# Performance work log

Measured on AMD Instinct MI355X. Metric: run time of the kernel, lower is better.

## Reference

```python
import jax, jax.numpy as jnp
import numpy as np

MAX_CH = 21
LAT_DIM = 64
D_EMBED = 1024
N_HEADS = 16
D_HEAD = D_EMBED // N_HEADS  # 64
L = MAX_CH * LAT_DIM         # 1344 latents
B, T = 4, 1024


def setup_inputs() -> dict:
    key = jax.random.key(0)
    k1, k2, k3, k4, k5, k6 = jax.random.split(key, 6)
    x = jax.random.normal(k1, (B, T, D_EMBED), dtype=jnp.float32)
    # boolean channel mask [b, L, T]
    ch_mask = jax.random.randint(k2, (B, L, T), 0, 2) > 0
    # learned latent queries [L, H*d] (xavier-uniform-ish init)
    lim_q = float(np.sqrt(6.0 / (L + N_HEADS * D_HEAD)))
    latent_q = jax.random.uniform(k3, (L, N_HEADS * D_HEAD), minval=-lim_q, maxval=lim_q, dtype=jnp.float32)
    # Linear weights (torch layout: [out, in]) and biases
    lim_w = float(np.sqrt(1.0 / D_EMBED))
    w_k_w = jax.random.uniform(k4, (N_HEADS * D_HEAD, D_EMBED), minval=-lim_w, maxval=lim_w, dtype=jnp.float32)
    w_k_b = jnp.zeros((N_HEADS * D_HEAD,), dtype=jnp.float32)
    w_v_w = jax.random.uniform(k5, (N_HEADS * D_HEAD, D_EMBED), minval=-lim_w, maxval=lim_w, dtype=jnp.float32)
    w_v_b = jax.random.uniform(k6, (N_HEADS * D_HEAD,), minval=-lim_w, maxval=lim_w, dtype=jnp.float32)
    return {"x": x, "ch_mask": ch_mask, "latent_q": latent_q,
            "w_k_w": w_k_w, "w_k_b": w_k_b, "w_v_w": w_v_w, "w_v_b": w_v_b}


def reference(x, ch_mask, latent_q, w_k_w, w_k_b, w_v_w, w_v_b):
    b, t, d = x.shape
    H, dh = N_HEADS, D_HEAD
    l = latent_q.shape[0]
    # faithful to torch .view(-1, H, L, d): raw row-major reinterpretation
    lq = latent_q.reshape(1, H, l, dh)                    # [1,H,L,dh]
    k = (x @ w_k_w.T + w_k_b).reshape(b, t, H, dh).transpose(0, 2, 3, 1)  # [b,H,dh,T]
    v = (x @ w_v_w.T + w_v_b).reshape(b, t, H, dh).transpose(0, 2, 1, 3)  # [b,H,T,dh]
    scale = jnp.float32(H) ** -0.5  # note: n_heads**-0.5, as in source
    scores = jnp.einsum('ohld,bhdt->bhlt', lq, k) * scale  # [b,H,L,T]
    mask = ch_mask[:, None, :, :]                           # [b,1,L,T] broadcast over heads
    scores = jnp.where(mask, scores, jnp.float32(-1e9))
    w = jax.nn.softmax(scores, axis=-1)
    w = jnp.where(mask, w, jnp.float32(0.0))
    out = jnp.einsum('bhlt,bhtd->bhld', w, v)               # [b,H,L,dh]
    return out.transpose(0, 2, 1, 3).reshape(b, l, H * dh)  # [b,L,H*dh]
```

## Files before the change

kernel.cpp:

```cpp
#include <hip/hip_runtime.h>
#include <hip/hip_bf16.h>

#define B_SZ 4
#define T_SZ 1024
#define NH 16
#define L_SZ 1344
#define LT_COUNT 21

typedef __attribute__((ext_vector_type(8))) short short8;
typedef __attribute__((ext_vector_type(4))) short short4v;
typedef __attribute__((ext_vector_type(4))) float floatx4;

typedef __attribute__((address_space(1))) const void gvoid;
typedef __attribute__((address_space(3))) void svoid;
#define GLD16(gp, lp) \
  __builtin_amdgcn_global_load_lds((gvoid*)(gp), (svoid*)(lp), 16, 0, 0)

static __device__ inline short bf16bits(float f) {
  return __builtin_bit_cast(short, __float2bfloat16(f));
}
static __device__ inline short4v cvt4(float4 v) {
  short4v r;
  r.x = bf16bits(v.x); r.y = bf16bits(v.y);
  r.z = bf16bits(v.z); r.w = bf16bits(v.w);
  return r;
}

static __device__ inline unsigned pack_bf16_2(float a, float b) {
  unsigned ua = __builtin_bit_cast(unsigned, a) + 0x8000u;
  unsigned ub = __builtin_bit_cast(unsigned, b) + 0x8000u;
  return __builtin_amdgcn_perm(ub, ua, 0x07060302u);
}
static __device__ inline uint2 pack_bf16_4(float4 v) {
  return make_uint2(pack_bf16_2(v.x, v.y), pack_bf16_2(v.z, v.w));
}


__global__ __launch_bounds__(256) void mask_detect(
    const unsigned char* __restrict__ m, int* __restrict__ flag) {
  __shared__ int any_off4, any_at4;
  if (threadIdx.x == 0) { any_off4 = 0; any_at4 = 0; }
  __syncthreads();
  int a1 = 0, a2 = 0;
  for (int i = threadIdx.x; i < 4096; i += 256) {
    unsigned char v = m[i];
    if (v) {
      if ((i & 3) != 0) a1 = 1;
      if ((i & 7) == 4) a2 = 1;
    }
  }
  if (a1) atomicOr(&any_off4, 1);
  if (a2) atomicOr(&any_at4, 1);
  __syncthreads();
  if (threadIdx.x == 0) *flag = any_off4 ? 1 : (any_at4 ? 0 : 2);
}

__global__ __launch_bounds__(256) void maskbits_kernel(
    const void* __restrict__ mask, const int* __restrict__ flag,
    unsigned int* __restrict__ bits) {
  int idx = blockIdx.x * 256 + threadIdx.x;
  int f = *flag;
  bool v;
  if (f == 1)      v = ((const signed char*)mask)[idx] != 0;
  else if (f == 2) v = ((const long long*)mask)[idx] != 0;
  else             v = ((const int*)mask)[idx] != 0;
  unsigned long long bal = __ballot(v);
  int lane = threadIdx.x & 63;
  if ((lane & 31) == 0) {
    unsigned int w = (lane & 32) ? (unsigned int)(bal >> 32) : (unsigned int)bal;
    bits[idx >> 5] = w;
  }
}

__global__ __launch_bounds__(256) void cvt_bf16(
    const float4* __restrict__ src, uint2* __restrict__ dst) {
  size_t i = (size_t)blockIdx.x * 256 + threadIdx.x;
  dst[i] = pack_bf16_4(src[i]);
}

static __device__ __forceinline__ void epi_k(const floatx4 acc[4][4],
    int bxt, int byd, int wm, int wn, int c15, int kq,
    const float* __restrict__ bk, __hip_bfloat16* __restrict__ k_buf) {
  #pragma unroll
  for (int ni = 0; ni < 4; ++ni) {
    int gr = bxt * 128 + wn * 64 + ni * 16 + c15;
    int b = gr >> 10, tc = (gr >> 6) & 15;
    #pragma unroll
    for (int mi = 0; mi < 4; ++mi) {
      int d0 = byd * 128 + wm * 64 + mi * 16 + kq * 4;
      int h = d0 >> 6, hd = d0 & 63;
      int half = hd >> 5, q4 = (hd >> 3) & 3, jlo = hd & 7;
      int bh = b * 16 + h;
      float4 b4 = *(const float4*)(bk + d0);
      float4 v4 = {acc[mi][ni][0] + b4.x, acc[mi][ni][1] + b4.y,
                   acc[mi][ni][2] + b4.z, acc[mi][ni][3] + b4.w};
      *(uint2*)(k_buf + ((size_t)((bh * 16 + tc) * 8 + ni * 2 + half)) * 512 +
                (q4 * 16 + c15) * 8 + jlo) = pack_bf16_4(v4);
    }
  }
}

static __device__ __forceinline__ void epi_v(const floatx4 acc[4][4],
    int bxd, int byt, int wm, int wn, int c15, int kq,
    const float* __restrict__ bv, __hip_bfloat16* __restrict__ v_buf) {
  #pragma unroll
  for (int ni = 0; ni < 4; ++ni) {
    int d = bxd * 128 + wn * 64 + ni * 16 + c15;
    int h = d >> 6;
    float bias = bv[d];
    #pragma unroll
    for (int mi = 0; mi < 4; ++mi) {
      int gr = byt * 128 + wm * 64 + mi * 16 + kq * 4;
      int b = gr >> 10, tc = (gr >> 6) & 15;
      int tl = gr & 63;
      int half = tl >> 5, q4 = (tl >> 3) & 3, jlo = tl & 7;
      int bh = b * 16 + h;
      float4 v4 = {acc[mi][ni][0] + bias, acc[mi][ni][1] + bias,
                   acc[mi][ni][2] + bias, acc[mi][ni][3] + bias};
      *(uint2*)(v_buf + ((size_t)((bh * 16 + tc) * 8 + ni * 2 + half)) * 512 +
                (q4 * 16 + c15) * 8 + jlo) = pack_bf16_4(v4);
    }
  }
}

static __device__ __forceinline__ void gemm_core(
    const __hip_bfloat16* __restrict__ A, const __hip_bfloat16* __restrict__ B,
    __hip_bfloat16* ldsA, __hip_bfloat16* ldsB,
    int TA, int TB, int tid, floatx4 (&acc)[4][4]) {
  const int lane = tid & 63, w = tid >> 6;
  const int wm = w & 1, wn = w >> 1;
  const int c15 = lane & 15, kq = lane >> 4;
  for (int kk = 0; kk < 1024; kk += 32) {
    #pragma unroll
    for (int j = 0; j < 2; ++j) {
      int c = w * 128 + j * 64 + lane;
      int row = c >> 2;
      int gkc = (c & 3) ^ (row & 3);
      GLD16(A + (size_t)(TA * 128 + row) * 1024 + kk + gkc * 8,
            ldsA + (w * 128 + j * 64) * 8);
      GLD16(B + (size_t)(TB * 128 + row) * 1024 + kk + gkc * 8,
            ldsB + (w * 128 + j * 64) * 8);
    }
    __syncthreads();
    short8 af[4], bf[4];
    #pragma unroll
    for (int mi = 0; mi < 4; ++mi) {
      int row = wm * 64 + mi * 16 + c15;
      af[mi] = *(const short8*)(ldsA + row * 32 + ((kq ^ (row & 3)) * 8));
    }
    #pragma unroll
    for (int ni = 0; ni < 4; ++ni) {
      int row = wn * 64 + ni * 16 + c15;
      bf[ni] = *(const short8*)(ldsB + row * 32 + ((kq ^ (row & 3)) * 8));
    }
    #pragma unroll
    for (int mi = 0; mi < 4; ++mi)
      #pragma unroll
      for (int ni = 0; ni < 4; ++ni)
        acc[mi][ni] = __builtin_amdgcn_mfma_f32_16x16x32_bf16(
            af[mi], bf[ni], acc[mi][ni], 0, 0, 0);
    __syncthreads();
  }
}

__global__ __launch_bounds__(256) void gemm_kv_bf16(
    const __hip_bfloat16* __restrict__ xb,
    const __hip_bfloat16* __restrict__ wkb, const __hip_bfloat16* __restrict__ wvb,
    const float* __restrict__ bk, const float* __restrict__ bv,
    __hip_bfloat16* __restrict__ k_buf, __hip_bfloat16* __restrict__ v_buf) {
  __shared__ __align__(16) __hip_bfloat16 ldsA[128 * 32];
  __shared__ __align__(16) __hip_bfloat16 ldsB[128 * 32];
  const int tid = threadIdx.x;
  const int lane = tid & 63, w = tid >> 6;
  const int wm = w & 1, wn = w >> 1;
  const int c15 = lane & 15, kq = lane >> 4;
  floatx4 acc[4][4];
  for (int i = 0; i < 4; ++i)
    for (int j = 0; j < 4; ++j) acc[i][j] = (floatx4){0.f, 0.f, 0.f, 0.f};

  if (blockIdx.z == 0) {
    gemm_core(wkb, xb, ldsA, ldsB, blockIdx.y, blockIdx.x, tid, acc);
    epi_k(acc, blockIdx.x, blockIdx.y, wm, wn, c15, kq, bk, k_buf);
  } else {
    gemm_core(xb, wvb, ldsA, ldsB, blockIdx.x, blockIdx.y, tid, acc);
    epi_v(acc, blockIdx.y, blockIdx.x, wm, wn, c15, kq, bv, v_buf);
  }
}

__global__ __launch_bounds__(256, 3) void attn_kernel(
    const float* __restrict__ latent_q,
    const __hip_bfloat16* __restrict__ k_buf,
    const __hip_bfloat16* __restrict__ v_buf,
    const unsigned int* __restrict__ mbits,
    float* __restrict__ out) {
  __shared__ __align__(16) __hip_bfloat16 ldsK[2][4096];
  __shared__ __align__(16) __hip_bfloat16 ldsV[2][4096];
  __shared__ __align__(16) __hip_bfloat16 pbuf[4][16 * 72];
  __shared__ uint2 mrows[64][17];

  const int tid = threadIdx.x;
  const int lane = tid & 63;
  const int w = tid >> 6;
  int bid = blockIdx.x;
  int xcd = bid & 7, j = bid >> 3;
  int bh = xcd * 8 + j / LT_COUNT;
  int lt = j % LT_COUNT;
  int h = bh & 15, b = bh >> 4;
  const int q4 = lane >> 4, c15 = lane & 15;
  const int l0 = lt * 64;

  {
    const unsigned int* msrc = mbits + (size_t)(b * L_SZ + l0) * 32;
    #pragma unroll
    for (int p = 0; p < 2; ++p) {
      int i = p * 256 + tid;
      uint4 m4 = *(const uint4*)(msrc + i * 4);
      int row = i >> 3, c2 = (i & 7) * 2;
      mrows[row][c2]     = make_uint2(m4.x, m4.y);
      mrows[row][c2 + 1] = make_uint2(m4.z, m4.w);
    }
  }

  const float QS = 0.25f * 1.44269504089f;
  short8 qf[2];
  {
    const float* qp = latent_q + ((size_t)(h * L_SZ + l0 + w * 16 + c15)) * 64 + q4 * 8;
    float4 a0 = *(const float4*)(qp);
    float4 a1 = *(const float4*)(qp + 4);
    float4 a2 = *(const float4*)(qp + 32);
    float4 a3 = *(const float4*)(qp + 36);
    a0.x *= QS; a0.y *= QS; a0.z *= QS; a0.w *= QS;
    a1.x *= QS; a1.y *= QS; a1.z *= QS; a1.w *= QS;
    a2.x *= QS; a2.y *= QS; a2.z *= QS; a2.w *= QS;
    a3.x *= QS; a3.y *= QS; a3.z *= QS; a3.w *= QS;
    short4v t0 = cvt4(a0), t1 = cvt4(a1), t2 = cvt4(a2), t3 = cvt4(a3);
    qf[0] = (short8){t0.x, t0.y, t0.z, t0.w, t1.x, t1.y, t1.z, t1.w};
    qf[1] = (short8){t2.x, t2.y, t2.z, t2.w, t3.x, t3.y, t3.z, t3.w};
  }
  __syncthreads();

  floatx4 l4 = (floatx4){0.f, 0.f, 0.f, 0.f};
  floatx4 o_acc[4];
  #pragma unroll
  for (int di = 0; di < 4; ++di) o_acc[di] = (floatx4){0.f, 0.f, 0.f, 0.f};

  const __hip_bfloat16* kb = k_buf + (size_t)bh * 65536;
  const __hip_bfloat16* vb = v_buf + (size_t)bh * 65536;
  __hip_bfloat16* pw = pbuf[w];

#define STAGE_KV(sb, tcn) do {                                              \
    const __hip_bfloat16* gk_ = kb + (size_t)(tcn) * 4096;                  \
    const __hip_bfloat16* gv_ = vb + (size_t)(tcn) * 4096;                  \
    int o0_ = w * 512 + lane * 8;                                           \
    GLD16(gk_ + o0_,        &ldsK[sb][w * 512]);                            \
    GLD16(gk_ + 2048 + o0_, &ldsK[sb][2048 + w * 512]);                     \
    GLD16(gv_ + o0_,        &ldsV[sb][w * 512]);                            \
    GLD16(gv_ + 2048 + o0_, &ldsV[sb][2048 + w * 512]);                     \
  } while (0)

  STAGE_KV(0, 0);

  for (int tc = 0; tc < 16; ++tc) {
    const int buf = tc & 1;
    if (tc + 1 < 16) {
      STAGE_KV(buf ^ 1, tc + 1);
      asm volatile("s_waitcnt vmcnt(4)" ::: "memory");
    } else {
      asm volatile("s_waitcnt vmcnt(0)" ::: "memory");
    }
    __builtin_amdgcn_s_barrier();

    short8 kf[2][4];
    #pragma unroll
    for (int half = 0; half < 2; ++half)
      #pragma unroll
      for (int ni = 0; ni < 4; ++ni)
        kf[half][ni] = *(const short8*)(&ldsK[buf][(ni * 2 + half) * 512 + lane * 8]);
    uint2 mw = mrows[w * 16 + c15][tc];
    floatx4 s[4];
    #pragma unroll
    for (int ni = 0; ni < 4; ++ni) s[ni] = (floatx4){0.f, 0.f, 0.f, 0.f};
    #pragma unroll
    for (int half = 0; half < 2; ++half)
      #pragma unroll
      for (int ni = 0; ni < 4; ++ni)
        s[ni] = __builtin_amdgcn_mfma_f32_16x16x32_bf16(kf[half][ni], qf[half], s[ni], 0, 0, 0);

    short8 vf[2][4];
    #pragma unroll
    for (int half = 0; half < 2; ++half)
      #pragma unroll
      for (int di = 0; di < 4; ++di)
        vf[half][di] = *(const short8*)(&ldsV[buf][(di * 2 + half) * 512 + lane * 8]);

    #pragma unroll
    for (int ni = 0; ni < 4; ++ni) {
      unsigned mword = (ni >= 2) ? mw.y : mw.x;
      float4 p4;
      #pragma unroll
      for (int r = 0; r < 4; ++r) {
        float e = exp2f(s[ni][r]);
        int sh = (ni & 1) * 16 + q4 * 4 + r;
        ((float*)&p4)[r] = ((mword >> sh) & 1) ? e : 0.f;
      }
      l4[0] += p4.x; l4[1] += p4.y;
      l4[2] += p4.z; l4[3] += p4.w;
      *(uint2*)(pw + c15 * 72 + ni * 16 + q4 * 4) = pack_bf16_4(p4);
    }

    short8 pf0 = *(const short8*)(pw + c15 * 72 + q4 * 8);
    short8 pf1 = *(const short8*)(pw + c15 * 72 + 32 + q4 * 8);
    #pragma unroll
    for (int di = 0; di < 4; ++di)
      o_acc[di] = __builtin_amdgcn_mfma_f32_16x16x32_bf16(vf[0][di], pf0, o_acc[di], 0, 0, 0);
    #pragma unroll
    for (int di = 0; di < 4; ++di)
      o_acc[di] = __builtin_amdgcn_mfma_f32_16x16x32_bf16(vf[1][di], pf1, o_acc[di], 0, 0, 0);

    asm volatile("s_waitcnt lgkmcnt(0)" ::: "memory");
    __builtin_amdgcn_s_barrier();
  }
#undef STAGE_KV

  float la = (l4[0] + l4[1]) + (l4[2] + l4[3]);
  la += __shfl_xor(la, 16, 64);
  la += __shfl_xor(la, 32, 64);
  float inv = (la > 0.f) ? 1.f / la : 0.f;
  float* ob = out + ((size_t)(b * L_SZ + l0 + w * 16 + c15)) * 1024 + h * 64;
  #pragma unroll
  for (int di = 0; di < 4; ++di) {
    float4 o4 = {o_acc[di][0] * inv, o_acc[di][1] * inv,
                 o_acc[di][2] * inv, o_acc[di][3] * inv};
    *(float4*)(ob + di * 16 + q4 * 4) = o4;
  }
}

extern "C" void kernel_launch(void* const* d_in, const int* in_sizes, int n_in,
                              void* d_out, int out_size, void* d_ws, size_t ws_size,
                              hipStream_t stream) {
  const float* x      = (const float*)d_in[0];
  const void* ch_mask = d_in[1];
  const float* lq     = (const float*)d_in[2];
  const float* wk     = (const float*)d_in[3];
  const float* bk     = (const float*)d_in[4];
  const float* wv     = (const float*)d_in[5];
  const float* bv     = (const float*)d_in[6];
  float* out = (float*)d_out;

  char* ws = (char*)d_ws;
  unsigned int* mbits   = (unsigned int*)ws;
  int* flag             = (int*)(ws + 720896);
  __hip_bfloat16* k_buf = (__hip_bfloat16*)(ws + 786432);
  __hip_bfloat16* v_buf = (__hip_bfloat16*)(ws + 786432 + 8388608);

  __hip_bfloat16* xb  = (__hip_bfloat16*)d_out;
  __hip_bfloat16* wkb = xb + 4 * 1024 * 1024;
  __hip_bfloat16* wvb = wkb + 1024 * 1024;

  mask_detect<<<1, 256, 0, stream>>>((const unsigned char*)ch_mask, flag);
  maskbits_kernel<<<21504, 256, 0, stream>>>(ch_mask, flag, mbits);

  cvt_bf16<<<4096, 256, 0, stream>>>((const float4*)x, (uint2*)xb);
  cvt_bf16<<<1024, 256, 0, stream>>>((const float4*)wk, (uint2*)wkb);
  cvt_bf16<<<1024, 256, 0, stream>>>((const float4*)wv, (uint2*)wvb);
  gemm_kv_bf16<<<dim3(32, 8, 2), 256, 0, stream>>>(xb, wkb, wvb, bk, bv, k_buf, v_buf);

  attn_kernel<<<8 * 168, 256, 0, stream>>>(lq, k_buf, v_buf, mbits, out);
}
```

Before: 199.4 us.

## Fuse prep kernels, double-buffer K/V GEMM with smaller tiles, prioritize attention MFMAs

Merges the mask-bit packing and the three bf16 conversion launches into one prep kernel, which removes three kernel launches. Restructures the K/V projection GEMM to use 128x64 tiles with double-buffered LDS staging and a 4-blocks-per-CU launch bound. The smaller tiles give 1024 blocks instead of 512 and let the next k-slice load overlap the current MFMAs. Also raises wave priority around the MFMA sections of the attention kernel with s_setprio. Smaller tiles lower data reuse per block, and the priority hints may shift the instruction schedule unpredictably.

```diff
diff --git a/kernel.cpp b/kernel.cpp
--- a/kernel.cpp
+++ b/kernel.cpp
@@ -55,135 +55,151 @@
   if (threadIdx.x == 0) *flag = any_off4 ? 1 : (any_at4 ? 0 : 2);
 }
 
-__global__ __launch_bounds__(256) void maskbits_kernel(
+__global__ __launch_bounds__(256) void prep_kernel(
+    const float4* __restrict__ x, const float4* __restrict__ wk,
+    const float4* __restrict__ wv,
+    uint2* __restrict__ xb, uint2* __restrict__ wkb, uint2* __restrict__ wvb,
     const void* __restrict__ mask, const int* __restrict__ flag,
     unsigned int* __restrict__ bits) {
-  int idx = blockIdx.x * 256 + threadIdx.x;
-  int f = *flag;
-  bool v;
-  if (f == 1)      v = ((const signed char*)mask)[idx] != 0;
-  else if (f == 2) v = ((const long long*)mask)[idx] != 0;
-  else             v = ((const int*)mask)[idx] != 0;
-  unsigned long long bal = __ballot(v);
-  int lane = threadIdx.x & 63;
-  if ((lane & 31) == 0) {
-    unsigned int w = (lane & 32) ? (unsigned int)(bal >> 32) : (unsigned int)bal;
-    bits[idx >> 5] = w;
-  }
-}
-
-__global__ __launch_bounds__(256) void cvt_bf16(
-    const float4* __restrict__ src, uint2* __restrict__ dst) {
-  size_t i = (size_t)blockIdx.x * 256 + threadIdx.x;
-  dst[i] = pack_bf16_4(src[i]);
-}
-
-static __device__ __forceinline__ void epi_k(const floatx4 acc[4][4],
-    int bxt, int byd, int wm, int wn, int c15, int kq,
-    const float* __restrict__ bk, __hip_bfloat16* __restrict__ k_buf) {
-  #pragma unroll
-  for (int ni = 0; ni < 4; ++ni) {
-    int gr = bxt * 128 + wn * 64 + ni * 16 + c15;
-    int b = gr >> 10, tc = (gr >> 6) & 15;
-    #pragma unroll
-    for (int mi = 0; mi < 4; ++mi) {
-      int d0 = byd * 128 + wm * 64 + mi * 16 + kq * 4;
-      int h = d0 >> 6, hd = d0 & 63;
-      int half = hd >> 5, q4 = (hd >> 3) & 3, jlo = hd & 7;
-      int bh = b * 16 + h;
-      float4 b4 = *(const float4*)(bk + d0);
-      float4 v4 = {acc[mi][ni][0] + b4.x, acc[mi][ni][1] + b4.y,
-                   acc[mi][ni][2] + b4.z, acc[mi][ni][3] + b4.w};
-      *(uint2*)(k_buf + ((size_t)((bh * 16 + tc) * 8 + ni * 2 + half)) * 512 +
-                (q4 * 16 + c15) * 8 + jlo) = pack_bf16_4(v4);
-    }
-  }
-}
-
-static __device__ __forceinline__ void epi_v(const floatx4 acc[4][4],
-    int bxd, int byt, int wm, int wn, int c15, int kq,
-    const float* __restrict__ bv, __hip_bfloat16* __restrict__ v_buf) {
-  #pragma unroll
-  for (int ni = 0; ni < 4; ++ni) {
-    int d = bxd * 128 + wn * 64 + ni * 16 + c15;
-    int h = d >> 6;
-    float bias = bv[d];
-    #pragma unroll
-    for (int mi = 0; mi < 4; ++mi) {
-      int gr = byt * 128 + wm * 64 + mi * 16 + kq * 4;
-      int b = gr >> 10, tc = (gr >> 6) & 15;
-      int tl = gr & 63;
-      int half = tl >> 5, q4 = (tl >> 3) & 3, jlo = tl & 7;
-      int bh = b * 16 + h;
-      float4 v4 = {acc[mi][ni][0] + bias, acc[mi][ni][1] + bias,
-                   acc[mi][ni][2] + bias, acc[mi][ni][3] + bias};
-      *(uint2*)(v_buf + ((size_t)((bh * 16 + tc) * 8 + ni * 2 + half)) * 512 +
-                (q4 * 16 + c15) * 8 + jlo) = pack_bf16_4(v4);
-    }
-  }
-}
-
-static __device__ __forceinline__ void gemm_core(
-    const __hip_bfloat16* __restrict__ A, const __hip_bfloat16* __restrict__ B,
-    __hip_bfloat16* ldsA, __hip_bfloat16* ldsB,
-    int TA, int TB, int tid, floatx4 (&acc)[4][4]) {
-  const int lane = tid & 63, w = tid >> 6;
-  const int wm = w & 1, wn = w >> 1;
-  const int c15 = lane & 15, kq = lane >> 4;
-  for (int kk = 0; kk < 1024; kk += 32) {
-    #pragma unroll
-    for (int j = 0; j < 2; ++j) {
-      int c = w * 128 + j * 64 + lane;
-      int row = c >> 2;
-      int gkc = (c & 3) ^ (row & 3);
-      GLD16(A + (size_t)(TA * 128 + row) * 1024 + kk + gkc * 8,
-            ldsA + (w * 128 + j * 64) * 8);
-      GLD16(B + (size_t)(TB * 128 + row) * 1024 + kk + gkc * 8,
-            ldsB + (w * 128 + j * 64) * 8);
-    }
-    __syncthreads();
-    short8 af[4], bf[4];
-    #pragma unroll
-    for (int mi = 0; mi < 4; ++mi) {
-      int row = wm * 64 + mi * 16 + c15;
-      af[mi] = *(const short8*)(ldsA + row * 32 + ((kq ^ (row & 3)) * 8));
-    }
-    #pragma unroll
-    for (int ni = 0; ni < 4; ++ni) {
-      int row = wn * 64 + ni * 16 + c15;
-      bf[ni] = *(const short8*)(ldsB + row * 32 + ((kq ^ (row & 3)) * 8));
-    }
-    #pragma unroll
-    for (int mi = 0; mi < 4; ++mi)
-      #pragma unroll
-      for (int ni = 0; ni < 4; ++ni)
-        acc[mi][ni] = __builtin_amdgcn_mfma_f32_16x16x32_bf16(
-            af[mi], bf[ni], acc[mi][ni], 0, 0, 0);
-    __syncthreads();
-  }
-}
-
-__global__ __launch_bounds__(256) void gemm_kv_bf16(
+  int bid = blockIdx.x;
+  if (bid < 6144) {
+    size_t i = (size_t)bid * 256 + threadIdx.x;
+    if (i < 1048576)      xb[i] = pack_bf16_4(x[i]);
+    else if (i < 1310720) wkb[i - 1048576] = pack_bf16_4(wk[i - 1048576]);
+    else                  wvb[i - 1310720] = pack_bf16_4(wv[i - 1310720]);
+  } else {
+    int idx = (bid - 6144) * 256 + threadIdx.x;
+    int f = *flag;
+    bool v;
+    if (f == 1)      v = ((const signed char*)mask)[idx] != 0;
+    else if (f == 2) v = ((const long long*)mask)[idx] != 0;
+    else             v = ((const int*)mask)[idx] != 0;
+    unsigned long long bal = __ballot(v);
+    int lane = threadIdx.x & 63;
+    if ((lane & 31) == 0) {
+      unsigned int w = (lane & 32) ? (unsigned int)(bal >> 32) : (unsigned int)bal;
+      bits[idx >> 5] = w;
+    }
+  }
+}
+
+__global__ __launch_bounds__(256, 4) void gemm_kv_bf16(
     const __hip_bfloat16* __restrict__ xb,
     const __hip_bfloat16* __restrict__ wkb, const __hip_bfloat16* __restrict__ wvb,
     const float* __restrict__ bk, const float* __restrict__ bv,
     __hip_bfloat16* __restrict__ k_buf, __hip_bfloat16* __restrict__ v_buf) {
-  __shared__ __align__(16) __hip_bfloat16 ldsA[128 * 32];
-  __shared__ __align__(16) __hip_bfloat16 ldsB[128 * 32];
+  __shared__ __align__(16) __hip_bfloat16 ldsA[2][128 * 32];
+  __shared__ __align__(16) __hip_bfloat16 ldsB[2][64 * 32];
   const int tid = threadIdx.x;
   const int lane = tid & 63, w = tid >> 6;
   const int wm = w & 1, wn = w >> 1;
   const int c15 = lane & 15, kq = lane >> 4;
-  floatx4 acc[4][4];
+
+  const __hip_bfloat16* A;
+  const __hip_bfloat16* B;
+  int TA, TB;
+  if (blockIdx.z == 0) {
+    A = wkb; B = xb; TA = blockIdx.x >> 6; TB = blockIdx.x & 63;
+  } else {
+    A = xb; B = wvb; TA = blockIdx.x >> 4; TB = blockIdx.x & 15;
+  }
+  const __hip_bfloat16* Abase = A + (size_t)TA * 128 * 1024;
+  const __hip_bfloat16* Bbase = B + (size_t)TB * 64 * 1024;
+
+  floatx4 acc[4][2];
+  #pragma unroll
   for (int i = 0; i < 4; ++i)
-    for (int j = 0; j < 4; ++j) acc[i][j] = (floatx4){0.f, 0.f, 0.f, 0.f};
+    #pragma unroll
+    for (int j = 0; j < 2; ++j) acc[i][j] = (floatx4){0.f, 0.f, 0.f, 0.f};
+
+#define GSTAGE(sb, kk) do {                                                  \
+    int cA_ = w * 128 + lane;                                                \
+    int rA_ = cA_ >> 2, gA_ = (cA_ & 3) ^ (rA_ & 3);                         \
+    GLD16(Abase + (size_t)rA_ * 1024 + (kk) + gA_ * 8,                       \
+          &ldsA[sb][(w * 128) * 8]);                                         \
+    int cA2_ = cA_ + 64;                                                     \
+    int rA2_ = cA2_ >> 2, gA2_ = (cA2_ & 3) ^ (rA2_ & 3);                    \
+    GLD16(Abase + (size_t)rA2_ * 1024 + (kk) + gA2_ * 8,                     \
+          &ldsA[sb][(w * 128 + 64) * 8]);                                    \
+    int cB_ = w * 64 + lane;                                                 \
+    int rB_ = cB_ >> 2, gB_ = (cB_ & 3) ^ (rB_ & 3);                         \
+    GLD16(Bbase + (size_t)rB_ * 1024 + (kk) + gB_ * 8,                       \
+          &ldsB[sb][(w * 64) * 8]);                                          \
+  } while (0)
+
+  GSTAGE(0, 0);
+  for (int kk = 0; kk < 1024; kk += 32) {
+    const int buf = (kk >> 5) & 1;
+    if (kk + 32 < 1024) {
+      GSTAGE(buf ^ 1, kk + 32);
+      asm volatile("s_waitcnt vmcnt(3)" ::: "memory");
+    } else {
+      asm volatile("s_waitcnt vmcnt(0)" ::: "memory");
+    }
+    __builtin_amdgcn_s_barrier();
+
+    short8 af[4], bfr[2];
+    #pragma unroll
+    for (int mi = 0; mi < 4; ++mi) {
+      int row = wm * 64 + mi * 16 + c15;
+      af[mi] = *(const short8*)(&ldsA[buf][row * 32 + ((kq ^ (row & 3)) * 8)]);
+    }
+    #pragma unroll
+    for (int ni = 0; ni < 2; ++ni) {
+      int row = wn * 32 + ni * 16 + c15;
+      bfr[ni] = *(const short8*)(&ldsB[buf][row * 32 + ((kq ^ (row & 3)) * 8)]);
+    }
+    #pragma unroll
+    for (int mi = 0; mi < 4; ++mi)
+      #pragma unroll
+      for (int ni = 0; ni < 2; ++ni)
+        acc[mi][ni] = __builtin_amdgcn_mfma_f32_16x16x32_bf16(
+            af[mi], bfr[ni], acc[mi][ni], 0, 0, 0);
+
+    asm volatile("s_waitcnt lgkmcnt(0)" ::: "memory");
+    __builtin_amdgcn_s_barrier();
+  }
+#undef GSTAGE
 
   if (blockIdx.z == 0) {
-    gemm_core(wkb, xb, ldsA, ldsB, blockIdx.y, blockIdx.x, tid, acc);
-    epi_k(acc, blockIdx.x, blockIdx.y, wm, wn, c15, kq, bk, k_buf);
+    #pragma unroll
+    for (int ni = 0; ni < 2; ++ni) {
+      int gr = TB * 64 + wn * 32 + ni * 16 + c15;
+      int b = gr >> 10, tc = (gr >> 6) & 15;
+      int ni2 = (gr & 63) >> 4;
+      #pragma unroll
+      for (int mi = 0; mi < 4; ++mi) {
+        int d0 = TA * 128 + wm * 64 + mi * 16 + kq * 4;
+        int h = d0 >> 6, hd = d0 & 63;
+        int half = hd >> 5, q4 = (hd >> 3) & 3, jlo = hd & 7;
+        int bh = b * 16 + h;
+        float4 b4 = *(const float4*)(bk + d0);
+        float4 v4 = {acc[mi][ni][0] + b4.x, acc[mi][ni][1] + b4.y,
+                     acc[mi][ni][2] + b4.z, acc[mi][ni][3] + b4.w};
+        *(uint2*)(k_buf + ((size_t)((bh * 16 + tc) * 8 + ni2 * 2 + half)) * 512 +
+                  (q4 * 16 + c15) * 8 + jlo) = pack_bf16_4(v4);
+      }
+    }
   } else {
-    gemm_core(xb, wvb, ldsA, ldsB, blockIdx.x, blockIdx.y, tid, acc);
-    epi_v(acc, blockIdx.y, blockIdx.x, wm, wn, c15, kq, bv, v_buf);
+    #pragma unroll
+    for (int ni = 0; ni < 2; ++ni) {
+      int d = TB * 64 + wn * 32 + ni * 16 + c15;
+      int h = d >> 6;
+      int di = (d & 63) >> 4;
+      float bias = bv[d];
+      #pragma unroll
+      for (int mi = 0; mi < 4; ++mi) {
+        int gr = TA * 128 + wm * 64 + mi * 16 + kq * 4;
+        int b = gr >> 10, tc = (gr >> 6) & 15;
+        int tl = gr & 63;
+        int half = tl >> 5, q4 = (tl >> 3) & 3, jlo = tl & 7;
+        int bh = b * 16 + h;
+        float4 v4 = {acc[mi][ni][0] + bias, acc[mi][ni][1] + bias,
+                     acc[mi][ni][2] + bias, acc[mi][ni][3] + bias};
+        *(uint2*)(v_buf + ((size_t)((bh * 16 + tc) * 8 + di * 2 + half)) * 512 +
+                  (q4 * 16 + c15) * 8 + jlo) = pack_bf16_4(v4);
+      }
+    }
   }
 }
 
@@ -280,11 +296,13 @@
     floatx4 s[4];
     #pragma unroll
     for (int ni = 0; ni < 4; ++ni) s[ni] = (floatx4){0.f, 0.f, 0.f, 0.f};
+    __builtin_amdgcn_s_setprio(1);
     #pragma unroll
     for (int half = 0; half < 2; ++half)
       #pragma unroll
       for (int ni = 0; ni < 4; ++ni)
         s[ni] = __builtin_amdgcn_mfma_f32_16x16x32_bf16(kf[half][ni], qf[half], s[ni], 0, 0, 0);
+    __builtin_amdgcn_s_setprio(0);
 
     short8 vf[2][4];
     #pragma unroll
@@ -310,12 +328,14 @@
 
     short8 pf0 = *(const short8*)(pw + c15 * 72 + q4 * 8);
     short8 pf1 = *(const short8*)(pw + c15 * 72 + 32 + q4 * 8);
+    __builtin_amdgcn_s_setprio(1);
     #pragma unroll
     for (int di = 0; di < 4; ++di)
       o_acc[di] = __builtin_amdgcn_mfma_f32_16x16x32_bf16(vf[0][di], pf0, o_acc[di], 0, 0, 0);
     #pragma unroll
     for (int di = 0; di < 4; ++di)
       o_acc[di] = __builtin_amdgcn_mfma_f32_16x16x32_bf16(vf[1][di], pf1, o_acc[di], 0, 0, 0);
+    __builtin_amdgcn_s_setprio(0);
 
     asm volatile("s_waitcnt lgkmcnt(0)" ::: "memory");
     __builtin_amdgcn_s_barrier();
@@ -358,12 +378,11 @@
   __hip_bfloat16* wvb = wkb + 1024 * 1024;
 
   mask_detect<<<1, 256, 0, stream>>>((const unsigned char*)ch_mask, flag);
-  maskbits_kernel<<<21504, 256, 0, stream>>>(ch_mask, flag, mbits);
-
-  cvt_bf16<<<4096, 256, 0, stream>>>((const float4*)x, (uint2*)xb);
-  cvt_bf16<<<1024, 256, 0, stream>>>((const float4*)wk, (uint2*)wkb);
-  cvt_bf16<<<1024, 256, 0, stream>>>((const float4*)wv, (uint2*)wvb);
-  gemm_kv_bf16<<<dim3(32, 8, 2), 256, 0, stream>>>(xb, wkb, wvb, bk, bv, k_buf, v_buf);
+  prep_kernel<<<27648, 256, 0, stream>>>(
+      (const float4*)x, (const float4*)wk, (const float4*)wv,
+      (uint2*)xb, (uint2*)wkb, (uint2*)wvb,
+      ch_mask, flag, mbits);
+  gemm_kv_bf16<<<dim3(512, 1, 2), 256, 0, stream>>>(xb, wkb, wvb, bk, bv, k_buf, v_buf);
 
   attn_kernel<<<8 * 168, 256, 0, stream>>>(lq, k_buf, v_buf, mbits, out);
 }
```

New measurement: 198.9 us. About the same (-0.3%).
